# Performance work log

Hardware: AMD Instinct MI355X
Metric: run time of the kernel (lower is better)

The kernel has to match this reference:

```python
import jax, jax.numpy as jnp
import numpy as np

N_NODES = 100000
N_EDGES = 1200000

def gcn_conv(x, edge_index, W, b, num_nodes):
    # PyG GCNConv with default normalize=True, add_self_loops=True.
    # x' = D^{-1/2} (A + I) D^{-1/2} X W + b, degrees on A + I.
    src, dst = edge_index[0], edge_index[1]
    loop = jnp.arange(num_nodes, dtype=edge_index.dtype)
    src = jnp.concatenate([src, loop])  # [E+N]
    dst = jnp.concatenate([dst, loop])
    deg = jax.ops.segment_sum(jnp.ones_like(dst, dtype=x.dtype), dst, num_segments=num_nodes)
    deg_inv_sqrt = jnp.where(deg > 0, jax.lax.rsqrt(deg), 0.0)
    norm = deg_inv_sqrt[src] * deg_inv_sqrt[dst]  # [E+N]
    xw = x @ W  # [N, out]
    msgs = norm[:, None] * xw[src]  # [E+N, out] gather
    out = jax.ops.segment_sum(msgs, dst, num_segments=num_nodes)  # scatter-add
    return out + b

def setup_inputs() -> dict:
    key = jax.random.key(0)
    ks = jax.random.split(key, 8)
    x = jax.random.normal(ks[0], (N_NODES, 26), dtype=jnp.float32)
    edge_index = jax.random.randint(ks[1], (2, N_EDGES), 0, N_NODES, dtype=jnp.int64)
    W1 = jax.random.normal(ks[2], (26, 64), dtype=jnp.float32) * 0.1
    b1 = jax.random.normal(ks[3], (64,), dtype=jnp.float32) * 0.1
    W2 = jax.random.normal(ks[4], (64, 32), dtype=jnp.float32) * 0.1
    b2 = jax.random.normal(ks[5], (32,), dtype=jnp.float32) * 0.1
    Wl = jax.random.normal(ks[6], (32, 1), dtype=jnp.float32) * 0.1
    bl = jax.random.normal(ks[7], (1,), dtype=jnp.float32) * 0.1
    return {"x": x, "edge_index": edge_index, "W1": W1, "b1": b1, "W2": W2, "b2": b2, "Wl": Wl, "bl": bl}

def reference(x, edge_index, W1, b1, W2, b2, Wl, bl):
    n = x.shape[0]
    h = gcn_conv(x, edge_index, W1, b1, n)
    h = jax.nn.relu(h)  # dropout is identity in eval mode
    h = gcn_conv(h, edge_index, W2, b2, n)
    h = jax.nn.relu(h)
    return h @ Wl + bl  # [N, 1]
```

## Files before the change

### kernel.cpp

```cpp
#include <hip/hip_runtime.h>
#include <hip/hip_fp16.h>


#define TPB 256
#define NPB 128
#define CAP 2048
#define EPB 4096
#define NBUCK_MAX 1024

typedef _Float16 half8 __attribute__((ext_vector_type(8)));
typedef float floatx4 __attribute__((ext_vector_type(4)));


__global__ __launch_bounds__(TPB) void scatter_direct_kernel(
        const int* __restrict__ src, const int* __restrict__ dst,
        int* __restrict__ bcnt, int* __restrict__ sortedb,
        const float* __restrict__ W1, const float* __restrict__ W2,
        float* __restrict__ W1t, float* __restrict__ W2t,
        int e, int nbuck) {
    __shared__ int lh[NBUCK_MAX];
    int t = threadIdx.x;
    for (int b = t; b < nbuck; b += TPB) lh[b] = 0;
    __syncthreads();
    int j0 = blockIdx.x * EPB;
    int j1 = min(e, j0 + EPB);
    for (int j = j0 + t; j < j1; j += TPB)
        atomicAdd(&lh[dst[j] >> 7], 1);
    __syncthreads();
    for (int b = t; b < nbuck; b += TPB) {
        int c = lh[b];
        int base = c ? atomicAdd(&bcnt[b], c) : 0;
        lh[b] = b * CAP + base;
    }
    __syncthreads();
    for (int j = j0 + t; j < j1; j += TPB) {
        int d = dst[j];
        int s = src[j];
        int pos = atomicAdd(&lh[d >> 7], 1);
        sortedb[pos] = (s << 7) | (d & 127);
    }
    if (blockIdx.x == 0) {
        for (int q = t; q < 64 * 32; q += TPB) {
            int f = q >> 5, k = q & 31;
            W1t[q] = (k < 26) ? W1[k * 64 + f] : 0.0f;
        }
        for (int q = t; q < 32 * 64; q += TPB) {
            int f = q >> 6, k = q & 63;
            W2t[q] = W2[k * 32 + f];
        }
    }
}


__global__ __launch_bounds__(TPB) void bucket_sort_fill_kernel(
        const int* __restrict__ sortedb, const int* __restrict__ bcnt,
        const float* __restrict__ x,
        int* __restrict__ slot, float* __restrict__ dis, int2* __restrict__ oe,
        __half* __restrict__ xs, int n, int nbuck) {
    __shared__ int c[NPB];
    __shared__ int ptr[NPB];
    __shared__ float sdis[NPB];
    int b = blockIdx.x, t = threadIdx.x;
    if (t < NPB) c[t] = 0;
    __syncthreads();
    int start = b * CAP;
    int end = start + bcnt[b];
    for (int j = start + t; j < end; j += TPB)
        atomicAdd(&c[sortedb[j] & 127], 1);
    __syncthreads();
    int mycnt = (t < NPB) ? c[t] : 0;
    for (int d = 1; d < NPB; d <<= 1) {
        int v = 0;
        if (t < NPB && t >= d) v = c[t - d];
        __syncthreads();
        if (t < NPB) c[t] += v;
        __syncthreads();
    }
    if (t < NPB) {
        int excl = c[t] - mycnt;
        ptr[t] = excl;
        float dv = rsqrtf((float)mycnt + 1.0f);
        sdis[t] = dv;
        int g = b * NPB + t;
        if (g < n) {
            dis[g] = dv;
            oe[g] = make_int2(start + excl, start + excl + mycnt);
        }
    }
    __syncthreads();
    for (int j = start + t; j < end; j += TPB) {
        int w = sortedb[j];
        int pos = atomicAdd(&ptr[w & 127], 1);
        slot[start + pos] = w >> 7;
    }
    int base = b * NPB;
    for (int i = t; i < NPB * 32; i += TPB) {
        int r = i >> 5, lane = i & 31;
        int g = base + r;
        if (g < n)
            xs[(size_t)g * 32 + lane] = __float2half(
                (lane < 26) ? sdis[r] * x[(size_t)g * 26 + lane] : 0.0f);
    }
}


__global__ __launch_bounds__(TPB) void gather1_dense_kernel(
        const __half* __restrict__ xs, const int2* __restrict__ oe,
        const int* __restrict__ slot, const float* __restrict__ dis,
        const float* __restrict__ W1t, const float* __restrict__ b1,
        const float* __restrict__ W2t, __half* __restrict__ xw2s, int n) {
    __shared__ _Float16 ssum[64][40];
    __shared__ _Float16 shh[4][16][72];
    __shared__ _Float16 sho[4][16][40];
    int t = threadIdx.x;
    int node0 = blockIdx.x * 64;
    const _Float16* xsp = (const _Float16*)xs;

    {
        int g = t >> 2;
        int fl = (t & 3) * 8;
        int node = node0 + g;
        float accf[8];
#pragma unroll
        for (int k = 0; k < 8; ++k) accf[k] = 0.0f;
        if (node < n) {
            half8 ownv = *(const half8*)(xsp + (size_t)node * 32 + fl);
#pragma unroll
            for (int k = 0; k < 8; ++k) accf[k] = (float)ownv[k];
            int2 se = oe[node];
            int j = se.x, end = se.y;
            for (; j + 3 < end; j += 4) {
                int s0 = slot[j], s1 = slot[j + 1], s2 = slot[j + 2], s3 = slot[j + 3];
                half8 v0 = *(const half8*)(xsp + (size_t)s0 * 32 + fl);
                half8 v1 = *(const half8*)(xsp + (size_t)s1 * 32 + fl);
                half8 v2 = *(const half8*)(xsp + (size_t)s2 * 32 + fl);
                half8 v3 = *(const half8*)(xsp + (size_t)s3 * 32 + fl);
#pragma unroll
                for (int k = 0; k < 8; ++k)
                    accf[k] += ((float)v0[k] + (float)v1[k]) + ((float)v2[k] + (float)v3[k]);
            }
            for (; j < end; ++j) {
                int s = slot[j];
                half8 v = *(const half8*)(xsp + (size_t)s * 32 + fl);
#pragma unroll
                for (int k = 0; k < 8; ++k) accf[k] += (float)v[k];
            }
        }
        half8 o;
#pragma unroll
        for (int k = 0; k < 8; ++k) o[k] = (_Float16)accf[k];
        *(half8*)&ssum[g][fl] = o;
    }
    __syncthreads();

    int w = t >> 6, l = t & 63;
    int tnode0 = node0 + w * 16;
    int lm = l & 15;
    int lk = l >> 4;

    half8 a1 = *(const half8*)&ssum[w * 16 + lm][lk * 8];

    float dvv[4];
#pragma unroll
    for (int r = 0; r < 4; ++r) {
        int nd = tnode0 + lk * 4 + r;
        dvv[r] = dis[nd < n ? nd : (n - 1)];
    }

#pragma unroll
    for (int T = 0; T < 4; ++T) {
        const float* bp = W1t + (size_t)(T * 16 + lm) * 32 + lk * 8;
        float4 bv0 = *(const float4*)bp;
        float4 bv1 = *(const float4*)(bp + 4);
        half8 bf;
        bf[0] = (_Float16)bv0.x; bf[1] = (_Float16)bv0.y;
        bf[2] = (_Float16)bv0.z; bf[3] = (_Float16)bv0.w;
        bf[4] = (_Float16)bv1.x; bf[5] = (_Float16)bv1.y;
        bf[6] = (_Float16)bv1.z; bf[7] = (_Float16)bv1.w;
        floatx4 c = {0.0f, 0.0f, 0.0f, 0.0f};
        c = __builtin_amdgcn_mfma_f32_16x16x32_f16(a1, bf, c, 0, 0, 0);
        float bias = b1[T * 16 + lm];
#pragma unroll
        for (int r = 0; r < 4; ++r) {
            float h = fmaxf(dvv[r] * c[r] + bias, 0.0f);
            shh[w][lk * 4 + r][T * 16 + lm] = (_Float16)h;
        }
    }

    half8 a2k0 = *(const half8*)&shh[w][lm][lk * 8];
    half8 a2k1 = *(const half8*)&shh[w][lm][32 + lk * 8];
#pragma unroll
    for (int T = 0; T < 2; ++T) {
        const float* bp0 = W2t + (size_t)(T * 16 + lm) * 64 + lk * 8;
        const float* bp1 = bp0 + 32;
        float4 c0 = *(const float4*)bp0;
        float4 c1 = *(const float4*)(bp0 + 4);
        float4 c2 = *(const float4*)bp1;
        float4 c3 = *(const float4*)(bp1 + 4);
        half8 bf0, bf1;
        bf0[0] = (_Float16)c0.x; bf0[1] = (_Float16)c0.y;
        bf0[2] = (_Float16)c0.z; bf0[3] = (_Float16)c0.w;
        bf0[4] = (_Float16)c1.x; bf0[5] = (_Float16)c1.y;
        bf0[6] = (_Float16)c1.z; bf0[7] = (_Float16)c1.w;
        bf1[0] = (_Float16)c2.x; bf1[1] = (_Float16)c2.y;
        bf1[2] = (_Float16)c2.z; bf1[3] = (_Float16)c2.w;
        bf1[4] = (_Float16)c3.x; bf1[5] = (_Float16)c3.y;
        bf1[6] = (_Float16)c3.z; bf1[7] = (_Float16)c3.w;
        floatx4 acc = {0.0f, 0.0f, 0.0f, 0.0f};
        acc = __builtin_amdgcn_mfma_f32_16x16x32_f16(a2k0, bf0, acc, 0, 0, 0);
        acc = __builtin_amdgcn_mfma_f32_16x16x32_f16(a2k1, bf1, acc, 0, 0, 0);
#pragma unroll
        for (int r = 0; r < 4; ++r)
            sho[w][lk * 4 + r][T * 16 + lm] = (_Float16)(dvv[r] * acc[r]);
    }

    int nl = l >> 2, fc = (l & 3) * 8;
    int gnode = tnode0 + nl;
    if (gnode < n) {
        half8 v = *(const half8*)&sho[w][nl][fc];
        *(half8*)((_Float16*)xw2s + (size_t)gnode * 32 + fc) = v;
    }
}


__global__ __launch_bounds__(TPB) void gather2_head_kernel(
        const __half* __restrict__ xw2s, const float* __restrict__ dis,
        const int2* __restrict__ oe, const int* __restrict__ slot,
        const float* __restrict__ b2, const float* __restrict__ Wl,
        const float* __restrict__ bl, float* __restrict__ out, int n) {
    int t = threadIdx.x;
    int g = t >> 2;
    int fl = (t & 3) * 8;
    int node = blockIdx.x * 64 + g;
    if (node >= n) return;
    const _Float16* xp = (const _Float16*)xw2s;

    float accf[8];
    half8 ownv = *(const half8*)(xp + (size_t)node * 32 + fl);
#pragma unroll
    for (int k = 0; k < 8; ++k) accf[k] = (float)ownv[k];
    int2 se = oe[node];
    int j = se.x, end = se.y;
    for (; j + 3 < end; j += 4) {
        int s0 = slot[j], s1 = slot[j + 1], s2 = slot[j + 2], s3 = slot[j + 3];
        half8 v0 = *(const half8*)(xp + (size_t)s0 * 32 + fl);
        half8 v1 = *(const half8*)(xp + (size_t)s1 * 32 + fl);
        half8 v2 = *(const half8*)(xp + (size_t)s2 * 32 + fl);
        half8 v3 = *(const half8*)(xp + (size_t)s3 * 32 + fl);
#pragma unroll
        for (int k = 0; k < 8; ++k)
            accf[k] += ((float)v0[k] + (float)v1[k]) + ((float)v2[k] + (float)v3[k]);
    }
    for (; j < end; ++j) {
        int s = slot[j];
        half8 v = *(const half8*)(xp + (size_t)s * 32 + fl);
#pragma unroll
        for (int k = 0; k < 8; ++k) accf[k] += (float)v[k];
    }

    float dv = dis[node];
    float4 bq0 = *(const float4*)(b2 + fl);
    float4 bq1 = *(const float4*)(b2 + fl + 4);
    float4 wq0 = *(const float4*)(Wl + fl);
    float4 wq1 = *(const float4*)(Wl + fl + 4);
    float bb[8] = {bq0.x, bq0.y, bq0.z, bq0.w, bq1.x, bq1.y, bq1.z, bq1.w};
    float wl[8] = {wq0.x, wq0.y, wq0.z, wq0.w, wq1.x, wq1.y, wq1.z, wq1.w};
    float c = 0.0f;
#pragma unroll
    for (int k = 0; k < 8; ++k) {
        float v = fmaxf(dv * accf[k] + bb[k], 0.0f);
        c += v * wl[k];
    }
    c += __shfl_xor(c, 1);
    c += __shfl_xor(c, 2);
    if ((t & 3) == 0) out[node] = c + bl[0];
}


extern "C" void kernel_launch(void* const* d_in, const int* in_sizes, int n_in,
                              void* d_out, int out_size, void* d_ws, size_t ws_size,
                              hipStream_t stream) {
    const float* x  = (const float*)d_in[0];
    const int*   ei = (const int*)d_in[1];
    const float* W1 = (const float*)d_in[2];
    const float* b1 = (const float*)d_in[3];
    const float* W2 = (const float*)d_in[4];
    const float* b2 = (const float*)d_in[5];
    const float* Wl = (const float*)d_in[6];
    const float* bl = (const float*)d_in[7];
    float* out = (float*)d_out;

    const int n = in_sizes[0] / 26;
    const int e = in_sizes[1] / 2;
    const int* src = ei;
    const int* dst = ei + e;

    const int nbuck = (n + NPB - 1) / NPB;
    const int eb    = (e + EPB - 1) / EPB;

    auto align_up = [](size_t v) { return (v + 255) & ~(size_t)255; };
    char* p = (char*)d_ws;
    int*    bcnt    = (int*)p;     p += align_up((size_t)nbuck * 4);
    int*    sortedb = (int*)p;     p += align_up(((size_t)nbuck * CAP + 4096) * 4);
    int*    slot    = (int*)p;     p += align_up(((size_t)nbuck * CAP + 4096) * 4);
    float*  dis     = (float*)p;   p += align_up((size_t)n * 4);
    int2*   oe      = (int2*)p;    p += align_up((size_t)n * 8);
    float*  W1t     = (float*)p;   p += align_up(64 * 32 * 4);
    float*  W2t     = (float*)p;   p += align_up(32 * 64 * 4);
    __half* xs      = (__half*)p;  p += align_up((size_t)n * 32 * 2);
    __half* xw2s    = (__half*)p;  p += align_up((size_t)n * 32 * 2);

    hipMemsetAsync(bcnt, 0, (size_t)nbuck * 4, stream);
    scatter_direct_kernel<<<eb, TPB, 0, stream>>>(src, dst, bcnt, sortedb,
                                                  W1, W2, W1t, W2t, e, nbuck);
    bucket_sort_fill_kernel<<<nbuck, TPB, 0, stream>>>(sortedb, bcnt, x, slot,
                                                       dis, oe, xs, n, nbuck);

    gather1_dense_kernel<<<(n + 63) / 64, TPB, 0, stream>>>(xs, oe, slot, dis,
                                                            W1t, b1, W2t, xw2s, n);

    gather2_head_kernel<<<(n + 63) / 64, TPB, 0, stream>>>(xw2s, dis, oe, slot,
                                                           b2, Wl, bl, out, n);
}
```

Measured before the change: 97.11 us.

## Pad per-node CSR segments to multiples of four and vectorize slot loads

Measured after the change: 98.57 us. No clear change (+1.5%).

```diff
diff --git a/kernel.cpp b/kernel.cpp
--- a/kernel.cpp
+++ b/kernel.cpp
@@ -4,7 +4,7 @@
 
 #define TPB 256
 #define NPB 128
-#define CAP 2048
+#define CAP 2176
 #define EPB 4096
 #define NBUCK_MAX 1024
 
@@ -24,8 +24,17 @@
     __syncthreads();
     int j0 = blockIdx.x * EPB;
     int j1 = min(e, j0 + EPB);
-    for (int j = j0 + t; j < j1; j += TPB)
-        atomicAdd(&lh[dst[j] >> 7], 1);
+    int pk[16], bk[16];
+#pragma unroll
+    for (int q = 0; q < 16; ++q) {
+        int j = j0 + t + q * TPB;
+        int valid = (j < j1);
+        int d = valid ? dst[j] : 0;
+        int s = valid ? src[j] : 0;
+        pk[q] = (s << 7) | (d & 127);
+        bk[q] = valid ? (d >> 7) : -1;
+        if (valid) atomicAdd(&lh[d >> 7], 1);
+    }
     __syncthreads();
     for (int b = t; b < nbuck; b += TPB) {
         int c = lh[b];
@@ -33,11 +42,12 @@
         lh[b] = b * CAP + base;
     }
     __syncthreads();
-    for (int j = j0 + t; j < j1; j += TPB) {
-        int d = dst[j];
-        int s = src[j];
-        int pos = atomicAdd(&lh[d >> 7], 1);
-        sortedb[pos] = (s << 7) | (d & 127);
+#pragma unroll
+    for (int q = 0; q < 16; ++q) {
+        if (bk[q] >= 0) {
+            int pos = atomicAdd(&lh[bk[q]], 1);
+            sortedb[pos] = pk[q];
+        }
     }
     if (blockIdx.x == 0) {
         for (int q = t; q < 64 * 32; q += TPB) {
@@ -69,6 +79,9 @@
         atomicAdd(&c[sortedb[j] & 127], 1);
     __syncthreads();
     int mycnt = (t < NPB) ? c[t] : 0;
+    int mypad = (mycnt + 3) & ~3;
+    if (t < NPB) c[t] = mypad;
+    __syncthreads();
     for (int d = 1; d < NPB; d <<= 1) {
         int v = 0;
         if (t < NPB && t >= d) v = c[t - d];
@@ -77,7 +90,7 @@
         __syncthreads();
     }
     if (t < NPB) {
-        int excl = c[t] - mycnt;
+        int excl = c[t] - mypad;
         ptr[t] = excl;
         float dv = rsqrtf((float)mycnt + 1.0f);
         sdis[t] = dv;
@@ -129,15 +142,32 @@
             for (int k = 0; k < 8; ++k) accf[k] = (float)ownv[k];
             int2 se = oe[node];
             int j = se.x, end = se.y;
-            for (; j + 3 < end; j += 4) {
-                int s0 = slot[j], s1 = slot[j + 1], s2 = slot[j + 2], s3 = slot[j + 3];
-                half8 v0 = *(const half8*)(xsp + (size_t)s0 * 32 + fl);
-                half8 v1 = *(const half8*)(xsp + (size_t)s1 * 32 + fl);
-                half8 v2 = *(const half8*)(xsp + (size_t)s2 * 32 + fl);
-                half8 v3 = *(const half8*)(xsp + (size_t)s3 * 32 + fl);
+            for (; j + 7 < end; j += 8) {
+                int4 sa = *(const int4*)(slot + j);
+                int4 sb = *(const int4*)(slot + j + 4);
+                half8 v0 = *(const half8*)(xsp + (size_t)sa.x * 32 + fl);
+                half8 v1 = *(const half8*)(xsp + (size_t)sa.y * 32 + fl);
+                half8 v2 = *(const half8*)(xsp + (size_t)sa.z * 32 + fl);
+                half8 v3 = *(const half8*)(xsp + (size_t)sa.w * 32 + fl);
+                half8 v4 = *(const half8*)(xsp + (size_t)sb.x * 32 + fl);
+                half8 v5 = *(const half8*)(xsp + (size_t)sb.y * 32 + fl);
+                half8 v6 = *(const half8*)(xsp + (size_t)sb.z * 32 + fl);
+                half8 v7 = *(const half8*)(xsp + (size_t)sb.w * 32 + fl);
+#pragma unroll
+                for (int k = 0; k < 8; ++k)
+                    accf[k] += (((float)v0[k] + (float)v1[k]) + ((float)v2[k] + (float)v3[k]))
+                             + (((float)v4[k] + (float)v5[k]) + ((float)v6[k] + (float)v7[k]));
+            }
+            if (j + 3 < end) {
+                int4 sa = *(const int4*)(slot + j);
+                half8 v0 = *(const half8*)(xsp + (size_t)sa.x * 32 + fl);
+                half8 v1 = *(const half8*)(xsp + (size_t)sa.y * 32 + fl);
+                half8 v2 = *(const half8*)(xsp + (size_t)sa.z * 32 + fl);
+                half8 v3 = *(const half8*)(xsp + (size_t)sa.w * 32 + fl);
 #pragma unroll
                 for (int k = 0; k < 8; ++k)
                     accf[k] += ((float)v0[k] + (float)v1[k]) + ((float)v2[k] + (float)v3[k]);
+                j += 4;
             }
             for (; j < end; ++j) {
                 int s = slot[j];
@@ -241,15 +271,32 @@
     for (int k = 0; k < 8; ++k) accf[k] = (float)ownv[k];
     int2 se = oe[node];
     int j = se.x, end = se.y;
-    for (; j + 3 < end; j += 4) {
-        int s0 = slot[j], s1 = slot[j + 1], s2 = slot[j + 2], s3 = slot[j + 3];
-        half8 v0 = *(const half8*)(xp + (size_t)s0 * 32 + fl);
-        half8 v1 = *(const half8*)(xp + (size_t)s1 * 32 + fl);
-        half8 v2 = *(const half8*)(xp + (size_t)s2 * 32 + fl);
-        half8 v3 = *(const half8*)(xp + (size_t)s3 * 32 + fl);
+    for (; j + 7 < end; j += 8) {
+        int4 sa = *(const int4*)(slot + j);
+        int4 sb = *(const int4*)(slot + j + 4);
+        half8 v0 = *(const half8*)(xp + (size_t)sa.x * 32 + fl);
+        half8 v1 = *(const half8*)(xp + (size_t)sa.y * 32 + fl);
+        half8 v2 = *(const half8*)(xp + (size_t)sa.z * 32 + fl);
+        half8 v3 = *(const half8*)(xp + (size_t)sa.w * 32 + fl);
+        half8 v4 = *(const half8*)(xp + (size_t)sb.x * 32 + fl);
+        half8 v5 = *(const half8*)(xp + (size_t)sb.y * 32 + fl);
+        half8 v6 = *(const half8*)(xp + (size_t)sb.z * 32 + fl);
+        half8 v7 = *(const half8*)(xp + (size_t)sb.w * 32 + fl);
+#pragma unroll
+        for (int k = 0; k < 8; ++k)
+            accf[k] += (((float)v0[k] + (float)v1[k]) + ((float)v2[k] + (float)v3[k]))
+                     + (((float)v4[k] + (float)v5[k]) + ((float)v6[k] + (float)v7[k]));
+    }
+    if (j + 3 < end) {
+        int4 sa = *(const int4*)(slot + j);
+        half8 v0 = *(const half8*)(xp + (size_t)sa.x * 32 + fl);
+        half8 v1 = *(const half8*)(xp + (size_t)sa.y * 32 + fl);
+        half8 v2 = *(const half8*)(xp + (size_t)sa.z * 32 + fl);
+        half8 v3 = *(const half8*)(xp + (size_t)sa.w * 32 + fl);
 #pragma unroll
         for (int k = 0; k < 8; ++k)
             accf[k] += ((float)v0[k] + (float)v1[k]) + ((float)v2[k] + (float)v3[k]);
+        j += 4;
     }
     for (; j < end; ++j) {
         int s = slot[j];
```

## Degree-sort nodes within 64-node groups to balance gather wavefronts; halve EPB

Applied to the files above, without the earlier changes.

After: 105.1 us. 1.08x slower.

```diff
diff --git a/kernel.cpp b/kernel.cpp
--- a/kernel.cpp
+++ b/kernel.cpp
@@ -5,7 +5,7 @@
 #define TPB 256
 #define NPB 128
 #define CAP 2048
-#define EPB 4096
+#define EPB 2048
 #define NBUCK_MAX 1024
 
 typedef _Float16 half8 __attribute__((ext_vector_type(8)));
@@ -56,10 +56,12 @@
         const int* __restrict__ sortedb, const int* __restrict__ bcnt,
         const float* __restrict__ x,
         int* __restrict__ slot, float* __restrict__ dis, int2* __restrict__ oe,
-        __half* __restrict__ xs, int n, int nbuck) {
+        __half* __restrict__ xs, int* __restrict__ perm, int n, int nbuck) {
     __shared__ int c[NPB];
     __shared__ int ptr[NPB];
     __shared__ float sdis[NPB];
+    __shared__ int skey[NPB];
+    __shared__ int sval[NPB];
     int b = blockIdx.x, t = threadIdx.x;
     if (t < NPB) c[t] = 0;
     __syncthreads();
@@ -101,25 +103,54 @@
             xs[(size_t)g * 32 + lane] = __float2half(
                 (lane < 26) ? sdis[r] * x[(size_t)g * 26 + lane] : 0.0f);
     }
+    if (t < NPB) { skey[t] = mycnt; sval[t] = t & 63; }
+    __syncthreads();
+    for (int k = 2; k <= 64; k <<= 1) {
+        for (int jj = k >> 1; jj > 0; jj >>= 1) {
+            if (t < NPB) {
+                int i = t & 63;
+                int ixj = i ^ jj;
+                if (ixj > i) {
+                    int h = t & 64;
+                    int a = h + i, bx = h + ixj;
+                    bool up = ((i & k) == 0);
+                    int ka = skey[a], kb = skey[bx];
+                    bool sw = up ? (ka < kb) : (ka > kb);
+                    if (sw) {
+                        skey[a] = kb; skey[bx] = ka;
+                        int va = sval[a]; sval[a] = sval[bx]; sval[bx] = va;
+                    }
+                }
+            }
+            __syncthreads();
+        }
+    }
+    if (t < NPB) perm[b * NPB + t] = b * NPB + (t & 64) + sval[t];
 }
 
 
 __global__ __launch_bounds__(TPB) void gather1_dense_kernel(
         const __half* __restrict__ xs, const int2* __restrict__ oe,
         const int* __restrict__ slot, const float* __restrict__ dis,
+        const int* __restrict__ perm,
         const float* __restrict__ W1t, const float* __restrict__ b1,
         const float* __restrict__ W2t, __half* __restrict__ xw2s, int n) {
     __shared__ _Float16 ssum[64][40];
     __shared__ _Float16 shh[4][16][72];
     __shared__ _Float16 sho[4][16][40];
+    __shared__ int sperm[64];
     int t = threadIdx.x;
     int node0 = blockIdx.x * 64;
     const _Float16* xsp = (const _Float16*)xs;
 
+    if (t < 64) sperm[t] = perm[node0 + t];
+    __syncthreads();
+
     {
         int g = t >> 2;
         int fl = (t & 3) * 8;
-        int node = node0 + g;
+        int node = sperm[g];
+        int nl = node - node0;
         float accf[8];
 #pragma unroll
         for (int k = 0; k < 8; ++k) accf[k] = 0.0f;
@@ -149,7 +180,7 @@
         half8 o;
 #pragma unroll
         for (int k = 0; k < 8; ++k) o[k] = (_Float16)accf[k];
-        *(half8*)&ssum[g][fl] = o;
+        *(half8*)&ssum[nl][fl] = o;
     }
     __syncthreads();
 
@@ -226,12 +257,17 @@
 __global__ __launch_bounds__(TPB) void gather2_head_kernel(
         const __half* __restrict__ xw2s, const float* __restrict__ dis,
         const int2* __restrict__ oe, const int* __restrict__ slot,
+        const int* __restrict__ perm,
         const float* __restrict__ b2, const float* __restrict__ Wl,
         const float* __restrict__ bl, float* __restrict__ out, int n) {
+    __shared__ int sperm[64];
     int t = threadIdx.x;
+    int node0 = blockIdx.x * 64;
+    if (t < 64) sperm[t] = perm[node0 + t];
+    __syncthreads();
     int g = t >> 2;
     int fl = (t & 3) * 8;
-    int node = blockIdx.x * 64 + g;
+    int node = sperm[g];
     if (node >= n) return;
     const _Float16* xp = (const _Float16*)xw2s;
 
@@ -305,6 +341,7 @@
     int*    slot    = (int*)p;     p += align_up(((size_t)nbuck * CAP + 4096) * 4);
     float*  dis     = (float*)p;   p += align_up((size_t)n * 4);
     int2*   oe      = (int2*)p;    p += align_up((size_t)n * 8);
+    int*    perm    = (int*)p;     p += align_up((size_t)nbuck * NPB * 4);
     float*  W1t     = (float*)p;   p += align_up(64 * 32 * 4);
     float*  W2t     = (float*)p;   p += align_up(32 * 64 * 4);
     __half* xs      = (__half*)p;  p += align_up((size_t)n * 32 * 2);
@@ -314,11 +351,11 @@
     scatter_direct_kernel<<<eb, TPB, 0, stream>>>(src, dst, bcnt, sortedb,
                                                   W1, W2, W1t, W2t, e, nbuck);
     bucket_sort_fill_kernel<<<nbuck, TPB, 0, stream>>>(sortedb, bcnt, x, slot,
-                                                       dis, oe, xs, n, nbuck);
-
-    gather1_dense_kernel<<<(n + 63) / 64, TPB, 0, stream>>>(xs, oe, slot, dis,
+                                                       dis, oe, xs, perm, n, nbuck);
+
+    gather1_dense_kernel<<<(n + 63) / 64, TPB, 0, stream>>>(xs, oe, slot, dis, perm,
                                                             W1t, b1, W2t, xw2s, n);
 
-    gather2_head_kernel<<<(n + 63) / 64, TPB, 0, stream>>>(xw2s, dis, oe, slot,
+    gather2_head_kernel<<<(n + 63) / 64, TPB, 0, stream>>>(xw2s, dis, oe, slot, perm,
                                                            b2, Wl, bl, out, n);
 }
```
